# Kernel tuning notes

Measured on AMD Instinct MI355X. Metric: run time of the kernel, lower is better.

Reference implementation:

```python
import jax, jax.numpy as jnp
import numpy as np

N_NODES = 50000
NEG_SLOPE = 0.2  # PyG GATConv default leaky_relu slope


def setup_inputs() -> dict:
    key = jax.random.key(0)
    ks = jax.random.split(key, 12)
    N, E, D_IN, H = N_NODES, 1200000, 128, 64
    sd_in = 1.0 / np.sqrt(D_IN)
    sd_h = 1.0 / np.sqrt(H)
    return {
        "x": jax.random.normal(ks[0], (N, D_IN), jnp.float32),
        "src": jax.random.randint(ks[1], (E,), 0, N, jnp.int32),
        "dst": jax.random.randint(ks[2], (E,), 0, N, jnp.int32),
        "W1_src": jax.random.normal(ks[3], (D_IN, H), jnp.float32) * sd_in,
        "W1_dst": jax.random.normal(ks[4], (D_IN, H), jnp.float32) * sd_in,
        "a1_src": jax.random.normal(ks[5], (H,), jnp.float32) * sd_h,
        "a1_dst": jax.random.normal(ks[6], (H,), jnp.float32) * sd_h,
        "b1": jnp.zeros((H,), jnp.float32),
        "W2_src": jax.random.normal(ks[7], (H, H), jnp.float32) * sd_h,
        "W2_dst": jax.random.normal(ks[8], (H, H), jnp.float32) * sd_h,
        "a2_src": jax.random.normal(ks[9], (H,), jnp.float32) * sd_h,
        "a2_dst": jax.random.normal(ks[10], (H,), jnp.float32) * sd_h,
        "b2": jnp.zeros((H,), jnp.float32),
    }


def _gat_layer(x, src, dst, W_src, W_dst, att_src, att_dst, bias):
    N = x.shape[0]
    h_src = x @ W_src            # [N, H] transformed source features
    h_dst = x @ W_dst            # [N, H] transformed destination features
    alpha_src = h_src @ att_src  # [N]
    alpha_dst = h_dst @ att_dst  # [N]
    # edge-wise attention logits (gather), edge j -> i: e = lrelu(a_src[j] + a_dst[i])
    e = jax.nn.leaky_relu(alpha_src[src] + alpha_dst[dst], NEG_SLOPE)  # [E]
    # segment softmax over incoming edges of each destination node
    m = jax.ops.segment_max(e, dst, num_segments=N)          # [N]
    ex = jnp.exp(e - m[dst])                                  # [E]
    denom = jax.ops.segment_sum(ex, dst, num_segments=N)     # [N]
    alpha = ex / denom[dst]                                   # [E]
    # weighted scatter-add aggregation
    msgs = h_src[src] * alpha[:, None]                        # [E, H]
    out = jax.ops.segment_sum(msgs, dst, num_segments=N)     # [N, H]
    return out + bias


def reference(x, src, dst, W1_src, W1_dst, a1_src, a1_dst, b1,
              W2_src, W2_dst, a2_src, a2_dst, b2):
    h = jnp.tanh(_gat_layer(x, src, dst, W1_src, W1_dst, a1_src, a1_dst, b1))
    h = jnp.tanh(_gat_layer(h, src, dst, W2_src, W2_dst, a2_src, a2_dst, b2))
    return h
```

## Files before the change

### kernel.cpp

```cpp
#include <hip/hip_runtime.h>
#include <hip/hip_bf16.h>

#define NEG_SLOPE 0.2f
#define EPB 4096
#define NHB 64

typedef __attribute__((ext_vector_type(8))) short short8v;
typedef __attribute__((ext_vector_type(4))) float f32x4;

__device__ inline float blo(unsigned u) { return __uint_as_float(u << 16); }
__device__ inline float bhi(unsigned u) { return __uint_as_float(u & 0xffff0000u); }
__device__ inline unsigned short bf16bits(float f) {
    __hip_bfloat16 b = __float2bfloat16(f);
    return *(unsigned short*)&b;
}
__device__ inline unsigned pack2bf(float e, float o) {
    return ((unsigned)bf16bits(o) << 16) | (unsigned)bf16bits(e);
}

template <int K>
__device__ inline void build_wt(unsigned short* __restrict__ Wt,
                                const float* __restrict__ W_src,
                                const float* __restrict__ a_src,
                                const float* __restrict__ W_dst,
                                const float* __restrict__ a_dst, int tid) {
    for (int i = tid; i < 64 * K; i += 256) {
        int k = i >> 6, j = i & 63;
        Wt[j * K + k] = bf16bits(W_src[i]);
    }
    for (int i = tid; i < 2 * K; i += 256) {
        int which = (i >= K) ? 1 : 0;
        int k = i - which * K;
        const float* Wr = (which ? W_dst : W_src) + k * 64;
        const float* av = which ? a_dst : a_src;
        float s = 0.f;
        #pragma unroll
        for (int j = 0; j < 64; ++j) s += Wr[j] * av[j];
        Wt[(64 + which) * K + k] = bf16bits(s);
    }
    for (int i = tid; i < 14 * K; i += 256) Wt[66 * K + i] = 0;
}

__global__ __launch_bounds__(256) void prep(
    const int* __restrict__ dst, int* __restrict__ partials, int E,
    const float* __restrict__ W1_src, const float* __restrict__ a1_src,
    const float* __restrict__ W1_dst, const float* __restrict__ a1_dst,
    const float* __restrict__ W2_src, const float* __restrict__ a2_src,
    const float* __restrict__ W2_dst, const float* __restrict__ a2_dst,
    unsigned short* __restrict__ Wt1, unsigned short* __restrict__ Wt2) {
    __shared__ int lh[256];
    int tid = threadIdx.x, b = blockIdx.x;
    if (b < NHB) {
        lh[tid] = 0;
        __syncthreads();
        for (int e = b * 256 + tid; e < E; e += NHB * 256)
            atomicAdd(&lh[dst[e] >> 8], 1);
        __syncthreads();
        partials[b * 256 + tid] = lh[tid];
    } else if (b == NHB) {
        build_wt<128>(Wt1, W1_src, a1_src, W1_dst, a1_dst, tid);
    } else {
        build_wt<64>(Wt2, W2_src, a2_src, W2_dst, a2_dst, tid);
    }
}

__global__ __launch_bounds__(256) void bucket_scan(const int* __restrict__ partials,
                                                   int* __restrict__ bucket_base,
                                                   int* __restrict__ bucket_cursor) {
    __shared__ int tmp[256];
    int tid = threadIdx.x;
    int v = 0;
    #pragma unroll 8
    for (int b = 0; b < NHB; ++b) v += partials[b * 256 + tid];
    tmp[tid] = v;
    __syncthreads();
    for (int off = 1; off < 256; off <<= 1) {
        int t = (tid >= off) ? tmp[tid - off] : 0;
        __syncthreads();
        tmp[tid] += t;
        __syncthreads();
    }
    int excl = tmp[tid] - v;
    bucket_base[tid] = excl;
    bucket_cursor[tid] = excl;
    if (tid == 255) bucket_base[256] = tmp[255];
}

__global__ __launch_bounds__(256) void bucket_scatter(const int* __restrict__ src,
                                                      const int* __restrict__ dst,
                                                      int* __restrict__ bucket_cursor,
                                                      unsigned* __restrict__ ebuf, int E) {
    __shared__ int lhist[256];
    __shared__ int lbase[256];
    int tid = threadIdx.x;
    lhist[tid] = 0;
    __syncthreads();
    int base = blockIdx.x * EPB;
    int bkt[16], rank[16];
    unsigned pack[16];
    #pragma unroll
    for (int i = 0; i < 16; ++i) {
        int e = base + i * 256 + tid;
        bkt[i] = -1;
        if (e < E) {
            int d = dst[e], s = src[e];
            bkt[i]  = d >> 8;
            pack[i] = ((unsigned)(d & 255) << 16) | (unsigned)s;
            rank[i] = atomicAdd(&lhist[bkt[i]], 1);
        }
    }
    __syncthreads();
    int cnt = lhist[tid];
    if (cnt) lbase[tid] = atomicAdd(&bucket_cursor[tid], cnt);
    __syncthreads();
    #pragma unroll
    for (int i = 0; i < 16; ++i)
        if (bkt[i] >= 0) ebuf[lbase[bkt[i]] + rank[i]] = pack[i];
}

__global__ __launch_bounds__(256) void bucket_build(const unsigned* __restrict__ ebuf,
                                                    const int* __restrict__ bucket_base,
                                                    int* __restrict__ row_ptr,
                                                    int* __restrict__ csr_src,
                                                    int N, int E) {
    __shared__ int deg[256];
    __shared__ int cur[256];
    __shared__ int tmp[256];
    int b = blockIdx.x, tid = threadIdx.x;
    int ebase = bucket_base[b], eend = bucket_base[b + 1];
    deg[tid] = 0;
    __syncthreads();
    for (int e = ebase + tid; e < eend; e += 256)
        atomicAdd(&deg[ebuf[e] >> 16], 1);
    __syncthreads();
    int v = deg[tid];
    tmp[tid] = v;
    __syncthreads();
    for (int off = 1; off < 256; off <<= 1) {
        int t = (tid >= off) ? tmp[tid - off] : 0;
        __syncthreads();
        tmp[tid] += t;
        __syncthreads();
    }
    int excl = tmp[tid] - v;
    int node = b * 256 + tid;
    if (node < N) row_ptr[node] = ebase + excl;
    if (b == 0 && tid == 0) row_ptr[N] = E;
    cur[tid] = excl;
    __syncthreads();
    for (int e = ebase + tid; e < eend; e += 256) {
        unsigned pk = ebuf[e];
        int r = atomicAdd(&cur[pk >> 16], 1);
        csr_src[ebase + r] = (int)(pk & 0xFFFFu);
    }
}

template <int K, bool INBF16>
__global__ __launch_bounds__(256) void nt_reg(
    const void* __restrict__ x_,
    const unsigned short* __restrict__ Wt,
    unsigned* __restrict__ hb_out,
    float* __restrict__ alpha_src, float* __restrict__ alpha_dst, int N) {
    int tid = threadIdx.x;
    int wid = tid >> 6, l = tid & 63;
    int rowbase = (blockIdx.x * 4 + wid) * 16;
    if (rowbase >= N) return;
    int jcol = l & 15, kg = (l >> 4) * 8;

    int r = rowbase + jcol;
    if (r >= N) r = N - 1;
    const float*          xr32 = (const float*)x_ + (size_t)r * K + kg;
    const unsigned short* xr16 = (const unsigned short*)x_ + (size_t)r * K + kg;

    f32x4 acc[5];
    #pragma unroll
    for (int t = 0; t < 5; ++t) acc[t] = (f32x4){0.f, 0.f, 0.f, 0.f};

    #pragma unroll
    for (int kt = 0; kt < K / 32; ++kt) {
        short8v a;
        if constexpr (INBF16) {
            a = *(const short8v*)(xr16 + kt * 32);
        } else {
            float4 xa = *(const float4*)(xr32 + kt * 32);
            float4 xb = *(const float4*)(xr32 + kt * 32 + 4);
            a[0] = (short)bf16bits(xa.x); a[1] = (short)bf16bits(xa.y);
            a[2] = (short)bf16bits(xa.z); a[3] = (short)bf16bits(xa.w);
            a[4] = (short)bf16bits(xb.x); a[5] = (short)bf16bits(xb.y);
            a[6] = (short)bf16bits(xb.z); a[7] = (short)bf16bits(xb.w);
        }
        int kbase = kt * 32 + kg;
        #pragma unroll
        for (int t = 0; t < 5; ++t) {
            short8v b = *(const short8v*)&Wt[(t * 16 + jcol) * K + kbase];
            acc[t] = __builtin_amdgcn_mfma_f32_16x16x32_bf16(a, b, acc[t], 0, 0, 0);
        }
    }

    int rbase = rowbase + (l >> 4) * 4;
    #pragma unroll
    for (int t = 0; t < 4; ++t) {
        #pragma unroll
        for (int rr = 0; rr < 4; ++rr) {
            float v = acc[t][rr];
            float w = __shfl_xor(v, 1);
            int row = rbase + rr;
            if (!(l & 1) && row < N)
                hb_out[(size_t)row * 32 + t * 8 + (jcol >> 1)] = pack2bf(v, w);
        }
    }
    #pragma unroll
    for (int rr = 0; rr < 4; ++rr) {
        int row = rbase + rr;
        if (row < N) {
            if (jcol == 0) alpha_src[row] = acc[4][rr];
            if (jcol == 1) alpha_dst[row] = acc[4][rr];
        }
    }
}

template <bool OUTBF16>
__global__ __launch_bounds__(256) void aggregate(
    const int* __restrict__ row_ptr, const int* __restrict__ csr_src,
    const float* __restrict__ alpha_src, const float* __restrict__ alpha_dst,
    const unsigned* __restrict__ hb,
    const float* __restrict__ bias,
    void* __restrict__ out_,
    int N) {
    int wid = threadIdx.x >> 6, lane = threadIdx.x & 63;
    int node = blockIdx.x * 4 + wid;
    if (node >= N) return;

    int beg = row_ptr[node], end = row_ptr[node + 1];
    float adst = alpha_dst[node];
    int half = lane >> 5, sub = lane & 31;

    float dL = 0.f;
    float aA[4] = {0.f, 0.f, 0.f, 0.f};
    float aB[4] = {0.f, 0.f, 0.f, 0.f};

    for (int c = beg; c < end; c += 64) {
        int cnt = end - c;
        cnt = (cnt < 64) ? cnt : 64;

        int s = 0;
        float p = 0.f;
        if (lane < cnt) {
            s = csr_src[c + lane];
            float t = alpha_src[s] + adst;
            t = (t > 0.f) ? t : NEG_SLOPE * t;
            p = __expf(fminf(t, 60.f));
            dL += p;
        }

        for (int j = 0; j < cnt; j += 16) {
            int   sv[8];
            float pv[8];
            unsigned uv[8];
            #pragma unroll
            for (int i = 0; i < 8; ++i) {
                int e = j + 2 * i + half;
                sv[i] = __shfl(s, e);
                pv[i] = __shfl(p, e);
            }
            #pragma unroll
            for (int i = 0; i < 8; ++i)
                uv[i] = hb[(size_t)sv[i] * 32 + sub];
            #pragma unroll
            for (int i = 0; i < 8; ++i) {
                aA[i & 3] = fmaf(pv[i], blo(uv[i]), aA[i & 3]);
                aB[i & 3] = fmaf(pv[i], bhi(uv[i]), aB[i & 3]);
            }
        }
    }
    float denom = dL;
    #pragma unroll
    for (int off = 32; off; off >>= 1) denom += __shfl_xor(denom, off);

    float accA = (aA[0] + aA[1]) + (aA[2] + aA[3]);
    float accB = (aB[0] + aB[1]) + (aB[2] + aB[3]);
    accA += __shfl_xor(accA, 32);
    accB += __shfl_xor(accB, 32);
    int srcl = lane >> 1;
    float vA = __shfl(accA, srcl);
    float vB = __shfl(accB, srcl);
    float val = (lane & 1) ? vB : vA;
    float r = (denom > 0.f) ? (val / denom) : 0.f;
    float fv = tanhf(r + bias[lane]);

    if constexpr (OUTBF16) {
        float fw = __shfl_xor(fv, 1);
        if (!(lane & 1))
            ((unsigned*)out_)[(size_t)node * 32 + (lane >> 1)] = pack2bf(fv, fw);
    } else {
        ((float*)out_)[(size_t)node * 64 + lane] = fv;
    }
}

extern "C" void kernel_launch(void* const* d_in, const int* in_sizes, int n_in,
                              void* d_out, int out_size, void* d_ws, size_t ws_size,
                              hipStream_t stream) {
    const float* x      = (const float*)d_in[0];
    const int*   src    = (const int*)  d_in[1];
    const int*   dst    = (const int*)  d_in[2];
    const float* W1_src = (const float*)d_in[3];
    const float* W1_dst = (const float*)d_in[4];
    const float* a1_src = (const float*)d_in[5];
    const float* a1_dst = (const float*)d_in[6];
    const float* b1     = (const float*)d_in[7];
    const float* W2_src = (const float*)d_in[8];
    const float* W2_dst = (const float*)d_in[9];
    const float* a2_src = (const float*)d_in[10];
    const float* a2_dst = (const float*)d_in[11];
    const float* b2     = (const float*)d_in[12];
    float* out = (float*)d_out;

    const int N = in_sizes[0] / 128;
    const int E = in_sizes[1];
    const int NB = (N + 255) / 256;

    char* ws = (char*)d_ws;
    size_t off = 0;
    auto alloc = [&](size_t bytes) {
        void* p = ws + off;
        off += (bytes + 255) & ~(size_t)255;
        return p;
    };
    unsigned* hbuf1  = (unsigned*)alloc((size_t)N * 32 * 4);
    unsigned* h1buf  = (unsigned*)alloc((size_t)N * 32 * 4);
    unsigned* hbuf2  = (unsigned*)alloc((size_t)N * 32 * 4);
    float* alpha_s1  = (float*)alloc((size_t)N * 4);
    float* alpha_d1  = (float*)alloc((size_t)N * 4);
    float* alpha_s2  = (float*)alloc((size_t)N * 4);
    float* alpha_d2  = (float*)alloc((size_t)N * 4);
    int*   row_ptr   = (int*)  alloc((size_t)(N + 1) * 4);
    int*   csr_src   = (int*)  alloc((size_t)E * 4);
    int*   partials  = (int*)  alloc(NHB * 256 * 4);
    int*   bucket_base   = (int*)alloc(257 * 4);
    int*   bucket_cursor = (int*)alloc(256 * 4);
    unsigned short* Wt1 = (unsigned short*)alloc(80 * 128 * 2);
    unsigned short* Wt2 = (unsigned short*)alloc(80 * 64 * 2);
    unsigned* ebuf   = (unsigned*)alloc((size_t)E * 4);
    (void)ws_size;

    const int eb3  = (E + EPB - 1) / EPB;
    const int nwb  = (N + 3) / 4;
    const int ntb  = (N + 63) / 64;

    prep<<<NHB + 2, 256, 0, stream>>>(dst, partials, E,
                                      W1_src, a1_src, W1_dst, a1_dst,
                                      W2_src, a2_src, W2_dst, a2_dst, Wt1, Wt2);
    bucket_scan<<<1, 256, 0, stream>>>(partials, bucket_base, bucket_cursor);
    bucket_scatter<<<eb3, 256, 0, stream>>>(src, dst, bucket_cursor, ebuf, E);
    bucket_build<<<NB, 256, 0, stream>>>(ebuf, bucket_base, row_ptr, csr_src, N, E);

    nt_reg<128, false><<<ntb, 256, 0, stream>>>(x, Wt1, hbuf1, alpha_s1, alpha_d1, N);
    aggregate<true><<<nwb, 256, 0, stream>>>(row_ptr, csr_src, alpha_s1, alpha_d1,
                                             hbuf1, b1, h1buf, N);
    nt_reg<64, true><<<ntb, 256, 0, stream>>>(h1buf, Wt2, hbuf2, alpha_s2, alpha_d2, N);
    aggregate<false><<<nwb, 256, 0, stream>>>(row_ptr, csr_src, alpha_s2, alpha_d2,
                                              hbuf2, b2, out, N);
}
```

Before: 144.4 us.

## Fuse bucket scan into scatter, merge layer-1 transform, split feature halves in aggregation

Removes the single-block bucket_scan launch by having each scatter and build block redo the small prefix scan over the partial histograms, with a zeroed cursor array. The layer-1 feature transform now runs as extra blocks of the scatter kernel, so CSR construction and the matmul can overlap. Node features are stored as two 32-column halves and each aggregate launch uses twice as many blocks, one half per block, to shrink the per-node gather footprint and raise parallelism. In exchange, every block repeats the partial-histogram scan, and the gathered edge lists and weights are read twice, once per half.

```diff
diff --git a/kernel.cpp b/kernel.cpp
--- a/kernel.cpp
+++ b/kernel.cpp
@@ -47,7 +47,8 @@
     const float* __restrict__ W1_dst, const float* __restrict__ a1_dst,
     const float* __restrict__ W2_src, const float* __restrict__ a2_src,
     const float* __restrict__ W2_dst, const float* __restrict__ a2_dst,
-    unsigned short* __restrict__ Wt1, unsigned short* __restrict__ Wt2) {
+    unsigned short* __restrict__ Wt1, unsigned short* __restrict__ Wt2,
+    int* __restrict__ cursor0) {
     __shared__ int lh[256];
     int tid = threadIdx.x, b = blockIdx.x;
     if (b < NHB) {
@@ -59,111 +60,40 @@
         partials[b * 256 + tid] = lh[tid];
     } else if (b == NHB) {
         build_wt<128>(Wt1, W1_src, a1_src, W1_dst, a1_dst, tid);
+    } else if (b == NHB + 1) {
+        build_wt<64>(Wt2, W2_src, a2_src, W2_dst, a2_dst, tid);
     } else {
-        build_wt<64>(Wt2, W2_src, a2_src, W2_dst, a2_dst, tid);
-    }
-}
-
-__global__ __launch_bounds__(256) void bucket_scan(const int* __restrict__ partials,
-                                                   int* __restrict__ bucket_base,
-                                                   int* __restrict__ bucket_cursor) {
-    __shared__ int tmp[256];
-    int tid = threadIdx.x;
+        cursor0[tid] = 0;
+    }
+}
+
+__device__ inline void local_scan(const int* __restrict__ partials,
+                                  int* sBase, int* sCnt, int tid) {
     int v = 0;
-    #pragma unroll 8
+    #pragma unroll
     for (int b = 0; b < NHB; ++b) v += partials[b * 256 + tid];
-    tmp[tid] = v;
+    sCnt[tid] = v;
+    sBase[tid] = v;
     __syncthreads();
     for (int off = 1; off < 256; off <<= 1) {
-        int t = (tid >= off) ? tmp[tid - off] : 0;
-        __syncthreads();
-        tmp[tid] += t;
-        __syncthreads();
-    }
-    int excl = tmp[tid] - v;
-    bucket_base[tid] = excl;
-    bucket_cursor[tid] = excl;
-    if (tid == 255) bucket_base[256] = tmp[255];
-}
-
-__global__ __launch_bounds__(256) void bucket_scatter(const int* __restrict__ src,
-                                                      const int* __restrict__ dst,
-                                                      int* __restrict__ bucket_cursor,
-                                                      unsigned* __restrict__ ebuf, int E) {
-    __shared__ int lhist[256];
-    __shared__ int lbase[256];
-    int tid = threadIdx.x;
-    lhist[tid] = 0;
-    __syncthreads();
-    int base = blockIdx.x * EPB;
-    int bkt[16], rank[16];
-    unsigned pack[16];
-    #pragma unroll
-    for (int i = 0; i < 16; ++i) {
-        int e = base + i * 256 + tid;
-        bkt[i] = -1;
-        if (e < E) {
-            int d = dst[e], s = src[e];
-            bkt[i]  = d >> 8;
-            pack[i] = ((unsigned)(d & 255) << 16) | (unsigned)s;
-            rank[i] = atomicAdd(&lhist[bkt[i]], 1);
-        }
-    }
-    __syncthreads();
-    int cnt = lhist[tid];
-    if (cnt) lbase[tid] = atomicAdd(&bucket_cursor[tid], cnt);
-    __syncthreads();
-    #pragma unroll
-    for (int i = 0; i < 16; ++i)
-        if (bkt[i] >= 0) ebuf[lbase[bkt[i]] + rank[i]] = pack[i];
-}
-
-__global__ __launch_bounds__(256) void bucket_build(const unsigned* __restrict__ ebuf,
-                                                    const int* __restrict__ bucket_base,
-                                                    int* __restrict__ row_ptr,
-                                                    int* __restrict__ csr_src,
-                                                    int N, int E) {
-    __shared__ int deg[256];
-    __shared__ int cur[256];
-    __shared__ int tmp[256];
-    int b = blockIdx.x, tid = threadIdx.x;
-    int ebase = bucket_base[b], eend = bucket_base[b + 1];
-    deg[tid] = 0;
-    __syncthreads();
-    for (int e = ebase + tid; e < eend; e += 256)
-        atomicAdd(&deg[ebuf[e] >> 16], 1);
-    __syncthreads();
-    int v = deg[tid];
-    tmp[tid] = v;
-    __syncthreads();
-    for (int off = 1; off < 256; off <<= 1) {
-        int t = (tid >= off) ? tmp[tid - off] : 0;
-        __syncthreads();
-        tmp[tid] += t;
-        __syncthreads();
-    }
-    int excl = tmp[tid] - v;
-    int node = b * 256 + tid;
-    if (node < N) row_ptr[node] = ebase + excl;
-    if (b == 0 && tid == 0) row_ptr[N] = E;
-    cur[tid] = excl;
-    __syncthreads();
-    for (int e = ebase + tid; e < eend; e += 256) {
-        unsigned pk = ebuf[e];
-        int r = atomicAdd(&cur[pk >> 16], 1);
-        csr_src[ebase + r] = (int)(pk & 0xFFFFu);
-    }
+        int t = (tid >= off) ? sBase[tid - off] : 0;
+        __syncthreads();
+        sBase[tid] += t;
+        __syncthreads();
+    }
+    sBase[tid] -= v;
+    __syncthreads();
 }
 
 template <int K, bool INBF16>
-__global__ __launch_bounds__(256) void nt_reg(
-    const void* __restrict__ x_,
-    const unsigned short* __restrict__ Wt,
-    unsigned* __restrict__ hb_out,
-    float* __restrict__ alpha_src, float* __restrict__ alpha_dst, int N) {
-    int tid = threadIdx.x;
+__device__ inline void nt_body(int nb, const void* __restrict__ x_,
+                               const unsigned short* __restrict__ Wt,
+                               unsigned* __restrict__ hb_lo,
+                               unsigned* __restrict__ hb_hi,
+                               float* __restrict__ alpha_src,
+                               float* __restrict__ alpha_dst, int N, int tid) {
     int wid = tid >> 6, l = tid & 63;
-    int rowbase = (blockIdx.x * 4 + wid) * 16;
+    int rowbase = (nb * 4 + wid) * 16;
     if (rowbase >= N) return;
     int jcol = l & 15, kg = (l >> 4) * 8;
 
@@ -200,13 +130,15 @@
     int rbase = rowbase + (l >> 4) * 4;
     #pragma unroll
     for (int t = 0; t < 4; ++t) {
+        unsigned* __restrict__ hb = (t < 2) ? hb_lo : hb_hi;
+        int toff = (t & 1) * 8;
         #pragma unroll
         for (int rr = 0; rr < 4; ++rr) {
             float v = acc[t][rr];
             float w = __shfl_xor(v, 1);
             int row = rbase + rr;
             if (!(l & 1) && row < N)
-                hb_out[(size_t)row * 32 + t * 8 + (jcol >> 1)] = pack2bf(v, w);
+                hb[(size_t)row * 16 + toff + (jcol >> 1)] = pack2bf(v, w);
         }
     }
     #pragma unroll
@@ -219,21 +151,107 @@
     }
 }
 
+__global__ __launch_bounds__(256) void scatter_nt1(
+    const int* __restrict__ src, const int* __restrict__ dst,
+    const int* __restrict__ partials, int* __restrict__ cursor0,
+    unsigned* __restrict__ ebuf, int E, int eb3,
+    const float* __restrict__ x, const unsigned short* __restrict__ Wt1,
+    unsigned* __restrict__ hb_lo, unsigned* __restrict__ hb_hi,
+    float* __restrict__ alpha_src, float* __restrict__ alpha_dst, int N) {
+    int tid = threadIdx.x;
+    if ((int)blockIdx.x >= eb3) {
+        nt_body<128, false>(blockIdx.x - eb3, x, Wt1, hb_lo, hb_hi,
+                            alpha_src, alpha_dst, N, tid);
+        return;
+    }
+    __shared__ int sBase[256];
+    __shared__ int sCnt[256];
+    __shared__ int lhist[256];
+    __shared__ int lbase[256];
+    local_scan(partials, sBase, sCnt, tid);
+
+    lhist[tid] = 0;
+    __syncthreads();
+    int base = blockIdx.x * EPB;
+    int bkt[16], rank[16];
+    unsigned pack[16];
+    #pragma unroll
+    for (int i = 0; i < 16; ++i) {
+        int e = base + i * 256 + tid;
+        bkt[i] = -1;
+        if (e < E) {
+            int d = dst[e], s = src[e];
+            bkt[i]  = d >> 8;
+            pack[i] = ((unsigned)(d & 255) << 16) | (unsigned)s;
+            rank[i] = atomicAdd(&lhist[bkt[i]], 1);
+        }
+    }
+    __syncthreads();
+    int cnt = lhist[tid];
+    if (cnt) lbase[tid] = sBase[tid] + atomicAdd(&cursor0[tid], cnt);
+    __syncthreads();
+    #pragma unroll
+    for (int i = 0; i < 16; ++i)
+        if (bkt[i] >= 0) ebuf[lbase[bkt[i]] + rank[i]] = pack[i];
+}
+
+__global__ __launch_bounds__(256) void bucket_build(
+    const unsigned* __restrict__ ebuf, const int* __restrict__ partials,
+    int* __restrict__ row_ptr, int* __restrict__ csr_src, int N, int E) {
+    __shared__ int sBase[256];
+    __shared__ int sCnt[256];
+    __shared__ int deg[256];
+    __shared__ int cur[256];
+    __shared__ int tmp[256];
+    int b = blockIdx.x, tid = threadIdx.x;
+    local_scan(partials, sBase, sCnt, tid);
+    int ebase = sBase[b], eend = sBase[b] + sCnt[b];
+
+    deg[tid] = 0;
+    __syncthreads();
+    for (int e = ebase + tid; e < eend; e += 256)
+        atomicAdd(&deg[ebuf[e] >> 16], 1);
+    __syncthreads();
+    int v = deg[tid];
+    tmp[tid] = v;
+    __syncthreads();
+    for (int off = 1; off < 256; off <<= 1) {
+        int t = (tid >= off) ? tmp[tid - off] : 0;
+        __syncthreads();
+        tmp[tid] += t;
+        __syncthreads();
+    }
+    int excl = tmp[tid] - v;
+    int node = b * 256 + tid;
+    if (node < N) row_ptr[node] = ebase + excl;
+    if (b == 0 && tid == 0) row_ptr[N] = E;
+    cur[tid] = excl;
+    __syncthreads();
+    for (int e = ebase + tid; e < eend; e += 256) {
+        unsigned pk = ebuf[e];
+        int r = atomicAdd(&cur[pk >> 16], 1);
+        csr_src[ebase + r] = (int)(pk & 0xFFFFu);
+    }
+}
+
 template <bool OUTBF16>
 __global__ __launch_bounds__(256) void aggregate(
     const int* __restrict__ row_ptr, const int* __restrict__ csr_src,
     const float* __restrict__ alpha_src, const float* __restrict__ alpha_dst,
-    const unsigned* __restrict__ hb,
+    const unsigned* __restrict__ hb_lo, const unsigned* __restrict__ hb_hi,
     const float* __restrict__ bias,
     void* __restrict__ out_,
-    int N) {
+    int N, int nwb) {
+    int half = ((int)blockIdx.x >= nwb) ? 1 : 0;
+    int bid = blockIdx.x - half * nwb;
     int wid = threadIdx.x >> 6, lane = threadIdx.x & 63;
-    int node = blockIdx.x * 4 + wid;
+    int node = bid * 4 + wid;
     if (node >= N) return;
 
     int beg = row_ptr[node], end = row_ptr[node + 1];
     float adst = alpha_dst[node];
-    int half = lane >> 5, sub = lane & 31;
+    int grp = lane >> 4, sub = lane & 15;
+    const unsigned* __restrict__ hbh = half ? hb_hi : hb_lo;
 
     float dL = 0.f;
     float aA[4] = {0.f, 0.f, 0.f, 0.f};
@@ -253,19 +271,19 @@
             dL += p;
         }
 
-        for (int j = 0; j < cnt; j += 16) {
+        for (int j = 0; j < cnt; j += 32) {
             int   sv[8];
             float pv[8];
             unsigned uv[8];
             #pragma unroll
             for (int i = 0; i < 8; ++i) {
-                int e = j + 2 * i + half;
+                int e = j + 4 * i + grp;
                 sv[i] = __shfl(s, e);
                 pv[i] = __shfl(p, e);
             }
             #pragma unroll
             for (int i = 0; i < 8; ++i)
-                uv[i] = hb[(size_t)sv[i] * 32 + sub];
+                uv[i] = hbh[(size_t)sv[i] * 16 + sub];
             #pragma unroll
             for (int i = 0; i < 8; ++i) {
                 aA[i & 3] = fmaf(pv[i], blo(uv[i]), aA[i & 3]);
@@ -276,25 +294,32 @@
     float denom = dL;
     #pragma unroll
     for (int off = 32; off; off >>= 1) denom += __shfl_xor(denom, off);
-
-    float accA = (aA[0] + aA[1]) + (aA[2] + aA[3]);
-    float accB = (aB[0] + aB[1]) + (aB[2] + aB[3]);
-    accA += __shfl_xor(accA, 32);
-    accB += __shfl_xor(accB, 32);
-    int srcl = lane >> 1;
-    float vA = __shfl(accA, srcl);
-    float vB = __shfl(accB, srcl);
-    float val = (lane & 1) ? vB : vA;
-    float r = (denom > 0.f) ? (val / denom) : 0.f;
-    float fv = tanhf(r + bias[lane]);
-
-    if constexpr (OUTBF16) {
-        float fw = __shfl_xor(fv, 1);
-        if (!(lane & 1))
-            ((unsigned*)out_)[(size_t)node * 32 + (lane >> 1)] = pack2bf(fv, fw);
-    } else {
-        ((float*)out_)[(size_t)node * 64 + lane] = fv;
-    }
+    float inv = (denom > 0.f) ? 1.f / denom : 0.f;
+
+    float A = (aA[0] + aA[1]) + (aA[2] + aA[3]);
+    float B = (aB[0] + aB[1]) + (aB[2] + aB[3]);
+    A += __shfl_xor(A, 16); A += __shfl_xor(A, 32);
+    B += __shfl_xor(B, 16); B += __shfl_xor(B, 32);
+
+    int f0 = half * 32 + 2 * sub;
+    float v0 = tanhf(A * inv + bias[f0]);
+    float v1 = tanhf(B * inv + bias[f0 + 1]);
+
+    if (grp == 0) {
+        if constexpr (OUTBF16) {
+            ((unsigned*)out_)[(size_t)node * 32 + half * 16 + sub] = pack2bf(v0, v1);
+        } else {
+            *(float2*)((float*)out_ + (size_t)node * 64 + f0) = make_float2(v0, v1);
+        }
+    }
+}
+
+__global__ __launch_bounds__(256) void nt2(
+    const unsigned short* __restrict__ x, const unsigned short* __restrict__ Wt,
+    unsigned* __restrict__ hb_lo, unsigned* __restrict__ hb_hi,
+    float* __restrict__ alpha_src, float* __restrict__ alpha_dst, int N) {
+    nt_body<64, true>(blockIdx.x, x, Wt, hb_lo, hb_hi, alpha_src, alpha_dst,
+                      N, threadIdx.x);
 }
 
 extern "C" void kernel_launch(void* const* d_in, const int* in_sizes, int n_in,
@@ -326,9 +351,11 @@
         off += (bytes + 255) & ~(size_t)255;
         return p;
     };
-    unsigned* hbuf1  = (unsigned*)alloc((size_t)N * 32 * 4);
+    unsigned* h1_lo  = (unsigned*)alloc((size_t)N * 16 * 4);
+    unsigned* h1_hi  = (unsigned*)alloc((size_t)N * 16 * 4);
     unsigned* h1buf  = (unsigned*)alloc((size_t)N * 32 * 4);
-    unsigned* hbuf2  = (unsigned*)alloc((size_t)N * 32 * 4);
+    unsigned* h2_lo  = (unsigned*)alloc((size_t)N * 16 * 4);
+    unsigned* h2_hi  = (unsigned*)alloc((size_t)N * 16 * 4);
     float* alpha_s1  = (float*)alloc((size_t)N * 4);
     float* alpha_d1  = (float*)alloc((size_t)N * 4);
     float* alpha_s2  = (float*)alloc((size_t)N * 4);
@@ -336,8 +363,7 @@
     int*   row_ptr   = (int*)  alloc((size_t)(N + 1) * 4);
     int*   csr_src   = (int*)  alloc((size_t)E * 4);
     int*   partials  = (int*)  alloc(NHB * 256 * 4);
-    int*   bucket_base   = (int*)alloc(257 * 4);
-    int*   bucket_cursor = (int*)alloc(256 * 4);
+    int*   cursor0   = (int*)  alloc(256 * 4);
     unsigned short* Wt1 = (unsigned short*)alloc(80 * 128 * 2);
     unsigned short* Wt2 = (unsigned short*)alloc(80 * 64 * 2);
     unsigned* ebuf   = (unsigned*)alloc((size_t)E * 4);
@@ -347,17 +373,18 @@
     const int nwb  = (N + 3) / 4;
     const int ntb  = (N + 63) / 64;
 
-    prep<<<NHB + 2, 256, 0, stream>>>(dst, partials, E,
+    prep<<<NHB + 3, 256, 0, stream>>>(dst, partials, E,
                                       W1_src, a1_src, W1_dst, a1_dst,
-                                      W2_src, a2_src, W2_dst, a2_dst, Wt1, Wt2);
-    bucket_scan<<<1, 256, 0, stream>>>(partials, bucket_base, bucket_cursor);
-    bucket_scatter<<<eb3, 256, 0, stream>>>(src, dst, bucket_cursor, ebuf, E);
-    bucket_build<<<NB, 256, 0, stream>>>(ebuf, bucket_base, row_ptr, csr_src, N, E);
-
-    nt_reg<128, false><<<ntb, 256, 0, stream>>>(x, Wt1, hbuf1, alpha_s1, alpha_d1, N);
-    aggregate<true><<<nwb, 256, 0, stream>>>(row_ptr, csr_src, alpha_s1, alpha_d1,
-                                             hbuf1, b1, h1buf, N);
-    nt_reg<64, true><<<ntb, 256, 0, stream>>>(h1buf, Wt2, hbuf2, alpha_s2, alpha_d2, N);
-    aggregate<false><<<nwb, 256, 0, stream>>>(row_ptr, csr_src, alpha_s2, alpha_d2,
-                                              hbuf2, b2, out, N);
-}
+                                      W2_src, a2_src, W2_dst, a2_dst,
+                                      Wt1, Wt2, cursor0);
+    scatter_nt1<<<eb3 + ntb, 256, 0, stream>>>(
+        src, dst, partials, cursor0, ebuf, E, eb3,
+        x, Wt1, h1_lo, h1_hi, alpha_s1, alpha_d1, N);
+    bucket_build<<<NB, 256, 0, stream>>>(ebuf, partials, row_ptr, csr_src, N, E);
+    aggregate<true><<<2 * nwb, 256, 0, stream>>>(
+        row_ptr, csr_src, alpha_s1, alpha_d1, h1_lo, h1_hi, b1, h1buf, N, nwb);
+    nt2<<<ntb, 256, 0, stream>>>((const unsigned short*)h1buf, Wt2,
+                                 h2_lo, h2_hi, alpha_s2, alpha_d2, N);
+    aggregate<false><<<2 * nwb, 256, 0, stream>>>(
+        row_ptr, csr_src, alpha_s2, alpha_d2, h2_lo, h2_hi, b2, out, N, nwb);
+}
```

Measured after the change: 162.6 us. +12.6%, slower.
